# Kernel optimization log

Measured on AMD Instinct MI355X. Metric: run time of the kernel, lower is better.

Reference implementation:

```python
import jax, jax.numpy as jnp
import numpy as np

K = 75        # kpoints
L = 8         # number of labels (output_dim)


def _knn_nonconformity(q, t, train_label, k=K, num_labels=L):
    """Brute-force kNN (Euclidean) + distance-weighted nonconformity.
    q: [B, D] queries; t: [N, D] train bank; train_label: [N] int.
    Returns [B, num_labels]: for each class i, sum of 1/dist over the k
    nearest neighbors whose label != i (0 weight for zero distance)."""
    # squared distances [B, N]
    d2 = (jnp.sum(q * q, axis=1, keepdims=True)
          - 2.0 * q @ t.T
          + jnp.sum(t * t, axis=1)[None, :])
    d2 = jnp.maximum(d2, 0.0)
    neg_top, idx = jax.lax.top_k(-d2, k)          # k smallest d2
    dist = jnp.sqrt(jnp.maximum(-neg_top, 0.0))    # [B, k]
    safe = jnp.where(dist > 0, dist, 1.0)
    w = jnp.where(dist > 0, 1.0 / safe, 0.0)       # [B, k]
    mismatch = 1.0 - jax.nn.one_hot(train_label[idx], num_labels, dtype=w.dtype)  # [B,k,L]
    return jnp.einsum('bk,bkl->bl', w, mismatch)


def setup_inputs() -> dict:
    key = jax.random.key(0)
    ks = jax.random.split(key, 12)
    B, N, D, H, C = 1024, 50000, 83, 128, 10000
    s = lambda fan_in: 1.0 / np.sqrt(fan_in)
    return {
        'x': jax.random.normal(ks[0], (B, D), jnp.float32),
        'train_x': jax.random.normal(ks[1], (N, D), jnp.float32),
        'train_label': jax.random.randint(ks[2], (N,), 0, L, jnp.int32),
        'cali': jax.random.uniform(ks[3], (C,), jnp.float32) * 50.0,
        'W1': jax.random.normal(ks[4], (D, H), jnp.float32) * s(D),
        'b1': jnp.zeros((H,), jnp.float32),
        'W2': jax.random.normal(ks[5], (H, H), jnp.float32) * s(H),
        'b2': jnp.zeros((H,), jnp.float32),
        'W3': jax.random.normal(ks[6], (H, H), jnp.float32) * s(H),
        'b3': jnp.zeros((H,), jnp.float32),
        'W4': jax.random.normal(ks[7], (H, L), jnp.float32) * s(H),
        'b4': jnp.zeros((L,), jnp.float32),
    }


def reference(x, train_x, train_label, cali, W1, b1, W2, b2, W3, b3, W4, b4):
    relu = jax.nn.relu
    # query-side MLP (inference: dropout inactive)
    h1 = relu(x @ W1 + b1)
    h2 = relu(h1 @ W2 + b2)
    h3 = relu(h2 @ W3 + b3)
    out = jax.nn.softmax(h3 @ W4 + b4, axis=-1)
    # train-side feature banks (what each kNTree was fit on)
    t1 = relu(train_x @ W1 + b1)
    t2 = relu(t1 @ W2 + b2)
    t3 = relu(t2 @ W3 + b3)
    t4 = jax.nn.softmax(t3 @ W4 + b4, axis=-1)
    # per-layer nonconformity [B, L], summed across the 5 layers
    total = (_knn_nonconformity(x, train_x, train_label)
             + _knn_nonconformity(h1, t1, train_label)
             + _knn_nonconformity(h2, t2, train_label)
             + _knn_nonconformity(h3, t3, train_label)
             + _knn_nonconformity(out, t4, train_label))
    # empirical p-value: fraction of calibration scores >= total nonconformity
    counts = jnp.sum(cali[None, None, :] >= total[:, :, None], axis=-1)  # [B, L]
    return counts.astype(jnp.float32) / cali.shape[0]
```

## Files before the change

kernel.cpp:

```cpp
#include <hip/hip_runtime.h>
#include <math.h>

#define KNN 75
#define NL 8
#define NB 1024
#define NT 50000
#define NT_PAD 50048
#define NCALI 10000
#define KC 32
#define TT 128
#define NTB 391
#define SLOTS 16
#define CAP 6144
#define NSUB 2048
#define NSB 16
#define SSTRIDE 24
#define SOFF 11
#define RSEL 32
#define MLP8_BQ 1563

#define PB_Q    384
#define PB_BANK 18750
#define PB_W1   48
#define PB_W23  64
#define PREP_BLOCKS (PB_Q+PB_BANK+PB_W1+2*PB_W23)

typedef __attribute__((ext_vector_type(8))) short bf16x8;
typedef __attribute__((ext_vector_type(4))) float f32x4;

__device__ __forceinline__ int swz(int c){ return c + ((c>>5)<<2); }

__device__ __forceinline__ unsigned short f2bf_rn(float x){
  unsigned u = __float_as_uint(x);
  unsigned r = (u + 0x7FFFu + ((u>>16)&1u)) >> 16;
  return (unsigned short)r;
}
__device__ __forceinline__ float bf2f(unsigned short h){
  return __uint_as_float(((unsigned)h)<<16);
}
__device__ __forceinline__ bf16x8 ld8(const unsigned short* p){
  return *(const bf16x8*)p;
}
__device__ __forceinline__ void gl_lds16(const unsigned short* g, unsigned short* l){
  __builtin_amdgcn_global_load_lds(
      (const __attribute__((address_space(1))) void*)g,
      (__attribute__((address_space(3))) void*)l, 16, 0, 0);
}

__device__ __forceinline__ void pad_one(const float* __restrict__ in,
                                        float* __restrict__ out, int M,
                                        int Din, int Dout, int idx){
  if (idx >= M*Dout) return;
  int r = idx / Dout, c = idx - r*Dout;
  out[idx] = (c < Din) ? in[r*Din + c] : 0.f;
}
__device__ __forceinline__ void wsplit_one(const float* __restrict__ W, int kreal,
                                           int dp, unsigned short* __restrict__ WtH,
                                           unsigned short* __restrict__ WtL, int idx){
  int n = idx / dp, k = idx - n*dp;
  float v = (k < kreal) ? W[(size_t)k*128 + n] : 0.f;
  unsigned short h = f2bf_rn(v);
  WtH[idx] = h;
  WtL[idx] = f2bf_rn(v - bf2f(h));
}
__global__ void prep_k(const float* __restrict__ x, float* __restrict__ xq0,
                       const float* __restrict__ txr, float* __restrict__ tbA,
                       const float* __restrict__ W1, unsigned short* wt1H, unsigned short* wt1L,
                       const float* __restrict__ W2, unsigned short* wt2H, unsigned short* wt2L,
                       const float* __restrict__ W3, unsigned short* wt3H, unsigned short* wt3L){
  int b = blockIdx.x, tid = threadIdx.x;
  if (b < PB_Q){
    pad_one(x, xq0, NB, 83, 96, b*256 + tid);
  } else if (b < PB_Q + PB_BANK){
    pad_one(txr, tbA, NT, 83, 96, (b-PB_Q)*256 + tid);
  } else if (b < PB_Q + PB_BANK + PB_W1){
    wsplit_one(W1, 83, 96,  wt1H, wt1L, (b-PB_Q-PB_BANK)*256 + tid);
  } else if (b < PB_Q + PB_BANK + PB_W1 + PB_W23){
    wsplit_one(W2, 128, 128, wt2H, wt2L, (b-PB_Q-PB_BANK-PB_W1)*256 + tid);
  } else {
    wsplit_one(W3, 128, 128, wt3H, wt3L, (b-PB_Q-PB_BANK-PB_W1-PB_W23)*256 + tid);
  }
}

__global__ void mlp8sm_k(const float* __restrict__ AB, const float* __restrict__ AQ,
                         const float* __restrict__ W4, const float* __restrict__ b4,
                         float* __restrict__ OutB,
                         unsigned short* __restrict__ SBH, unsigned short* __restrict__ SBL,
                         float* __restrict__ nrmB,
                         float* __restrict__ OutQ,
                         unsigned short* __restrict__ SQH, unsigned short* __restrict__ SQL,
                         float* __restrict__ nrmQ){
  __shared__ float Ws[128*8];
  int tid = threadIdx.x;
  for (int i=tid;i<1024;i+=256) Ws[i]=W4[i];
  __syncthreads();
  int b = blockIdx.x;
  bool isq = (b >= MLP8_BQ);
  int r = (isq ? (b-MLP8_BQ) : b)*32 + (tid>>3), c = tid&7;
  int M = isq ? NB : NT;
  if (r >= M) return;
  const float* A = isq ? AQ : AB;
  float* Out = isq ? OutQ : OutB;
  unsigned short* SH = isq ? SQH : SBH;
  unsigned short* SL = isq ? SQL : SBL;
  float* nrm = isq ? nrmQ : nrmB;
  const float* a = &A[(size_t)r*128];
  float acc = b4[c];
  #pragma unroll 16
  for (int k=0;k<128;k++) acc += a[k]*Ws[k*8+c];
  int lane = tid & 63, base = lane & ~7;
  float v[8];
  #pragma unroll
  for (int j=0;j<8;j++) v[j] = __shfl(acc, base+j, 64);
  float m=-1e30f;
  #pragma unroll
  for (int j=0;j<8;j++) m = v[j]>m ? v[j] : m;
  float s=0.f;
  #pragma unroll
  for (int j=0;j<8;j++){ v[j]=__expf(v[j]-m); s+=v[j]; }
  float inv=1.f/s;
  float nn=0.f;
  #pragma unroll
  for (int j=0;j<8;j++){ float pv=v[j]*inv; v[j]=pv; nn+=pv*pv; }
  float* p = &Out[(size_t)r*32];
  float pv = v[c];
  p[c]    = pv;
  p[8+c]  = 0.f;
  p[16+c] = 0.f;
  p[24+c] = 0.f;
  unsigned short h = f2bf_rn(pv);
  SH[(size_t)r*32 + c]    = h;
  SL[(size_t)r*32 + c]    = f2bf_rn(pv - bf2f(h));
  SH[(size_t)r*32 + 8+c]  = 0; SL[(size_t)r*32 + 8+c]  = 0;
  SH[(size_t)r*32 + 16+c] = 0; SL[(size_t)r*32 + 16+c] = 0;
  SH[(size_t)r*32 + 24+c] = 0; SL[(size_t)r*32 + 24+c] = 0;
  if (c==0) nrm[r] = nn;
}

__global__ void conv_norm_k(
    const float* __restrict__ XA, unsigned short* __restrict__ HA,
    unsigned short* __restrict__ LA, float* __restrict__ nA, int MA,
    const float* __restrict__ XB, unsigned short* __restrict__ HB,
    unsigned short* __restrict__ LB, float* __restrict__ nB, int MB,
    int dp)
{
  int w = threadIdx.x>>6, lane = threadIdx.x&63;
  int row = blockIdx.x*4 + w;
  const float* src; unsigned short* dh; unsigned short* dl; float* nrm;
  if (row < MA){
    src=&XA[(size_t)row*dp]; dh=&HA[(size_t)row*dp]; dl=&LA[(size_t)row*dp]; nrm=&nA[row];
  } else {
    int r2 = row - MA;
    if (r2 >= MB) return;
    src=&XB[(size_t)r2*dp]; dh=&HB[(size_t)r2*dp]; dl=&LB[(size_t)r2*dp]; nrm=&nB[r2];
  }
  float s=0.f;
  for (int c=lane*2; c<dp; c+=128){
    float2 v = *(const float2*)&src[c];
    s += v.x*v.x + v.y*v.y;
    unsigned short h0 = f2bf_rn(v.x), h1 = f2bf_rn(v.y);
    float r0 = v.x - bf2f(h0), r1 = v.y - bf2f(h1);
    ushort2 hh; hh.x=h0; hh.y=h1;
    ushort2 ll; ll.x=f2bf_rn(r0); ll.y=f2bf_rn(r1);
    *(ushort2*)&dh[c]=hh;
    *(ushort2*)&dl[c]=ll;
  }
  #pragma unroll
  for (int off=32;off>0;off>>=1) s += __shfl_down(s, off, 64);
  if (lane==0) *nrm=s;
}

__device__ __forceinline__ void find_bin(int* hist, int* part, int nb, int Krem,
                                         int tid, int* s_B, int* s_lob){
  int ch = nb>>8;
  int base = tid*ch;
  int s=0;
  for (int b=base;b<base+ch;b++) s+=hist[b];
  int lane = tid & 63, wv = tid>>6;
  int v = s;
  #pragma unroll
  for (int off=1; off<64; off<<=1){
    int u = __shfl_up(v, off, 64);
    if (lane >= off) v += u;
  }
  if (lane==63) part[wv] = v;
  __syncthreads();
  int wbase = 0;
  #pragma unroll
  for (int w2=0; w2<4; w2++) wbase += (w2 < wv) ? part[w2] : 0;
  v += wbase;
  int excl = v - s;
  if (v >= Krem && excl < Krem){
    int lob = excl, B = base + ch - 1;
    for (int b=base;b<base+ch;b++){
      if (lob + hist[b] >= Krem){ B=b; break; }
      lob += hist[b];
    }
    *s_B = B; *s_lob = lob;
  }
  if (tid==255 && v < Krem){ *s_B = nb-1; *s_lob = 0; }
  __syncthreads();
}

__global__ __launch_bounds__(256) void sel64_k(const unsigned* __restrict__ skeys,
                                               unsigned* __restrict__ Tthr){
  __shared__ unsigned buf[NSUB];
  __shared__ int hist[2048];
  __shared__ int part[256];
  __shared__ int sB, sLob;
  int tid=threadIdx.x, q=blockIdx.x;
  for (int i=tid;i<NSUB;i+=256) buf[i]=skeys[(size_t)q*NSUB+i];
  int Krem=RSEL;
  for (int i=tid;i<2048;i+=256) hist[i]=0;
  __syncthreads();
  for (int i=tid;i<NSUB;i+=256) atomicAdd(&hist[buf[i]>>21],1);
  __syncthreads();
  find_bin(hist,part,2048,Krem,tid,&sB,&sLob);
  unsigned pre=(unsigned)sB; Krem-=sLob;
  for (int i=tid;i<2048;i+=256) hist[i]=0;
  __syncthreads();
  for (int i=tid;i<NSUB;i+=256){ unsigned k=buf[i]; if ((k>>21)==pre) atomicAdd(&hist[(k>>10)&0x7FFu],1); }
  __syncthreads();
  find_bin(hist,part,2048,Krem,tid,&sB,&sLob);
  pre=(pre<<11)|(unsigned)sB; Krem-=sLob;
  for (int i=tid;i<1024;i+=256) hist[i]=0;
  __syncthreads();
  for (int i=tid;i<NSUB;i+=256){ unsigned k=buf[i]; if ((k>>10)==pre) atomicAdd(&hist[k&0x3FFu],1); }
  __syncthreads();
  find_bin(hist,part,1024,Krem,tid,&sB,&sLob);
  if (tid==0) Tthr[q]=(pre<<10)|(unsigned)sB;
}

#define MFMA_SEC(BHC, BLC, AH, AL)                                               \
  _Pragma("unroll")                                                              \
  for (int tj=0;tj<8;tj++){                                                      \
    int rowB = tj*16 + col;                                                      \
    int sw = (((quad + (rowB>>1)) & 3) << 3);                                    \
    bf16x8 bh = *(const bf16x8*)&(BHC)[rowB*32 + sw];                            \
    bf16x8 bl = *(const bf16x8*)&(BLC)[rowB*32 + sw];                            \
    acc[tj] = __builtin_amdgcn_mfma_f32_16x16x32_bf16(AH, bh, acc[tj], 0,0,0);   \
    acc[tj] = __builtin_amdgcn_mfma_f32_16x16x32_bf16(AH, bl, acc[tj], 0,0,0);   \
    acc[tj] = __builtin_amdgcn_mfma_f32_16x16x32_bf16(AL, bh, acc[tj], 0,0,0);   \
  }

#define MFMA_KLOOP(ROWMAP)                                                       \
  size_t aoff = (size_t)(qbase + w*16 + col)*dp + quad*8;                        \
  const unsigned short* pAH = QH + aoff;                                         \
  const unsigned short* pAL = QL + aoff;                                         \
  int i0 = tid,      row0 = i0>>2, sg0 = ((i0&3) - (row0>>1)) & 3;               \
  int i1 = tid+256,  row1 = i1>>2, sg1 = ((i1&3) - (row1>>1)) & 3;               \
  size_t g0 = (size_t)(ROWMAP(n0+row0))*dp + (size_t)sg0*8;                      \
  size_t g1 = (size_t)(ROWMAP(n0+row1))*dp + (size_t)sg1*8;                      \
  f32x4 acc[8];                                                                  \
  _Pragma("unroll")                                                              \
  for (int tj=0;tj<8;tj++){ f32x4 z={0.f,0.f,0.f,0.f}; acc[tj]=z; }              \
  gl_lds16(TH + g0, BH0 + i0*8);                                                 \
  gl_lds16(TH + g1, BH0 + i1*8);                                                 \
  gl_lds16(TL + g0, BL0 + i0*8);                                                 \
  gl_lds16(TL + g1, BL0 + i1*8);                                                 \
  bf16x8 xh = ld8(pAH), xl = ld8(pAL);                                           \
  bf16x8 yh = xh, yl = xl;                                                       \
  _Pragma("unroll")                                                              \
  for (int kc=0; kc<kchunks; kc+=2){                                             \
    __syncthreads();                                                             \
    if (kc+1 < kchunks){                                                         \
      size_t ko=(size_t)(kc+1)*32;                                               \
      gl_lds16(TH + g0 + ko, BH1 + i0*8);                                        \
      gl_lds16(TH + g1 + ko, BH1 + i1*8);                                        \
      gl_lds16(TL + g0 + ko, BL1 + i0*8);                                        \
      gl_lds16(TL + g1 + ko, BL1 + i1*8);                                        \
      yh = ld8(pAH + ko); yl = ld8(pAL + ko);                                    \
    }                                                                            \
    MFMA_SEC(BH0, BL0, xh, xl);                                                  \
    if (kc+1 < kchunks){                                                         \
      __syncthreads();                                                           \
      if (kc+2 < kchunks){                                                       \
        size_t ko=(size_t)(kc+2)*32;                                             \
        gl_lds16(TH + g0 + ko, BH0 + i0*8);                                      \
        gl_lds16(TH + g1 + ko, BH0 + i1*8);                                      \
        gl_lds16(TL + g0 + ko, BL0 + i0*8);                                      \
        gl_lds16(TL + g1 + ko, BL0 + i1*8);                                      \
        xh = ld8(pAH + ko); xl = ld8(pAL + ko);                                  \
      }                                                                          \
      MFMA_SEC(BH1, BL1, yh, yl);                                                \
    }                                                                            \
  }

#define ROW_ID(r) (r)
#define ROW_SUB(r) ((r)*SSTRIDE + SOFF)

template<int KCH>
__global__ __launch_bounds__(256) void dist_mfma_k(
    const unsigned short* __restrict__ QH, const unsigned short* __restrict__ QL,
    const unsigned short* __restrict__ TH, const unsigned short* __restrict__ TL,
    const float* __restrict__ qn, const float* __restrict__ tn,
    const int* __restrict__ labels, const unsigned* __restrict__ Tthr,
    unsigned* __restrict__ slab)
{
  constexpr int dp = KCH*32;
  __shared__ __align__(16) unsigned short smem[4*4096];
  unsigned short* BH0 = smem;
  unsigned short* BH1 = smem + 4096;
  unsigned short* BL0 = smem + 8192;
  unsigned short* BL1 = smem + 12288;
  unsigned (*hitbuf)[SLOTS] = (unsigned (*)[SLOTS])smem;
  int* hcnt = (int*)(smem + 4096);
  int b = blockIdx.x;
  int xcd = b & 7, s = b >> 3;
  int qb = s & 15, tslot = s >> 4;
  int t_blk = xcd + 8*tslot;
  if (t_blk >= NTB) return;
  int tid = threadIdx.x, w = tid>>6, lane = tid&63;
  int quad = lane>>4, col = lane&15;
  int qbase = qb*64;
  int n0 = t_blk*TT;
  constexpr int kchunks = KCH;

  MFMA_KLOOP(ROW_ID)

  __syncthreads();
  if (tid<64) hcnt[tid]=0;
  __syncthreads();
  float qnr[4]; unsigned Tq[4]; float thrF[4];
  #pragma unroll
  for (int r=0;r<4;r++){
    int q = qbase + w*16 + quad*4 + r;
    qnr[r]  = qn[q];
    Tq[r]   = Tthr[q];
    thrF[r] = __uint_as_float(Tq[r] | 7u);
  }
  #pragma unroll
  for (int tj=0;tj<8;tj++){
    int t = n0 + tj*16 + col;
    if (t < NT){
      float tnv = tn[t];
      unsigned lab = (unsigned)labels[t];
      #pragma unroll
      for (int r=0;r<4;r++){
        float d2 = fmaf(-2.f, acc[tj][r], qnr[r] + tnv);
        if (d2 <= thrF[r]){
          float d2c = fmaxf(d2, 0.f);
          unsigned key = (__float_as_uint(d2c)&0xFFFFFFF8u) | lab;
          if (key < Tq[r]){
            int ql = w*16 + quad*4 + r;
            int idx = atomicAdd(&hcnt[ql], 1);
            if (idx < SLOTS-1) hitbuf[ql][1+idx] = key;
          }
        }
      }
    }
  }
  __syncthreads();
  if (tid<64) hitbuf[tid][0]=(unsigned)hcnt[tid];
  __syncthreads();
  {
    int q = tid>>2, sub = (tid&3)*4;
    uint4 v = *(uint4*)&hitbuf[q][sub];
    *(uint4*)&slab[((size_t)(qbase+q)*NTB + t_blk)*SLOTS + sub] = v;
  }
}

template<int KCH>
__global__ __launch_bounds__(256) void dist_sub_k(
    const unsigned short* __restrict__ QH, const unsigned short* __restrict__ QL,
    const unsigned short* __restrict__ TH, const unsigned short* __restrict__ TL,
    const float* __restrict__ qn, const float* __restrict__ tn,
    const int* __restrict__ labels, unsigned* __restrict__ keys)
{
  constexpr int dp = KCH*32;
  __shared__ __align__(16) unsigned short smem[4*4096];
  unsigned short* BH0 = smem;
  unsigned short* BH1 = smem + 4096;
  unsigned short* BL0 = smem + 8192;
  unsigned short* BL1 = smem + 12288;
  int b = blockIdx.x;
  int qb = b & 15, t_blk = b >> 4;
  int tid = threadIdx.x, w = tid>>6, lane = tid&63;
  int quad = lane>>4, col = lane&15;
  int qbase = qb*64;
  int n0 = t_blk*TT;
  constexpr int kchunks = KCH;

  MFMA_KLOOP(ROW_SUB)

  float qnr[4];
  #pragma unroll
  for (int r=0;r<4;r++)
    qnr[r] = qn[qbase + w*16 + quad*4 + r];
  #pragma unroll
  for (int tj=0;tj<8;tj++){
    int sI = n0 + tj*16 + col;
    int g  = sI*SSTRIDE + SOFF;
    float tnv = tn[g];
    unsigned lab = (unsigned)labels[g];
    #pragma unroll
    for (int r=0;r<4;r++){
      float d2 = fmaxf(fmaf(-2.f, acc[tj][r], qnr[r] + tnv), 0.f);
      unsigned key = (__float_as_uint(d2)&0xFFFFFFF8u) | lab;
      int q = qbase + w*16 + quad*4 + r;
      keys[(size_t)q*NSUB + sI] = key;
    }
  }
}

template<int KCH>
__global__ __launch_bounds__(256) void mlp_mfma_k(
    const unsigned short* __restrict__ bkH, const unsigned short* __restrict__ bkL,
    const unsigned short* __restrict__ qh,  const unsigned short* __restrict__ ql,
    const unsigned short* __restrict__ TH, const unsigned short* __restrict__ TL,
    const float* __restrict__ bias,
    float* __restrict__ OutB, unsigned short* __restrict__ SBH,
    unsigned short* __restrict__ SBL, float* __restrict__ nrmB,
    float* __restrict__ OutQ, unsigned short* __restrict__ SQH,
    unsigned short* __restrict__ SQL, float* __restrict__ nrmQ)
{
  constexpr int dp = KCH*32;
  __shared__ __align__(16) unsigned short smem[4*4096];
  unsigned short* BH0 = smem;
  unsigned short* BH1 = smem + 4096;
  unsigned short* BL0 = smem + 8192;
  unsigned short* BL1 = smem + 12288;
  int b = blockIdx.x;
  bool isq = (b >= 2*NTB);
  const unsigned short* QH = isq ? qh : bkH;
  const unsigned short* QL = isq ? ql : bkL;
  float* Out = isq ? OutQ : OutB;
  unsigned short* SH = isq ? SQH : SBH;
  unsigned short* SL = isq ? SQL : SBL;
  float* nrm = isq ? nrmQ : nrmB;
  int M = isq ? NB : NT;
  int tid = threadIdx.x, w = tid>>6, lane = tid&63;
  int quad = lane>>4, col = lane&15;
  int qbase = (isq ? (b - 2*NTB) : b) * 64;
  int n0 = 0;
  constexpr int kchunks = KCH;

  MFMA_KLOOP(ROW_ID)

  float bb[8];
  #pragma unroll
  for (int tj=0;tj<8;tj++) bb[tj] = bias[tj*16 + col];
  #pragma unroll
  for (int r=0;r<4;r++){
    int row = qbase + w*16 + quad*4 + r;
    if (row < M){
      float vv[8]; float s=0.f;
      #pragma unroll
      for (int tj=0;tj<8;tj++){
        float v = acc[tj][r] + bb[tj];
        v = v > 0.f ? v : 0.f;
        vv[tj] = v;
        s += v*v;
        Out[(size_t)row*128 + tj*16 + col] = v;
      }
      #pragma unroll
      for (int off=1; off<16; off<<=1) s += __shfl_xor(s, off, 16);
      if (col==0) nrm[row] = s;
      #pragma unroll
      for (int tj=0;tj<8;tj++){
        unsigned short h = f2bf_rn(vv[tj]);
        SH[(size_t)row*128 + tj*16 + col] = h;
        SL[(size_t)row*128 + tj*16 + col] = f2bf_rn(vv[tj] - bf2f(h));
      }
    }
  }
}

__global__ __launch_bounds__(256) void final_k(
    const unsigned* __restrict__ slab,
    const float* __restrict__ Qm, const float* __restrict__ Tm,
    const float* __restrict__ qn, const float* __restrict__ tn,
    const int* __restrict__ labels,
    float* __restrict__ tot, int first, int dp)
{
  __shared__ int hist[2048];
  __shared__ int part[256];
  __shared__ unsigned buf[CAP];
  __shared__ unsigned lowbuf[96];
  __shared__ float qrow[128];
  __shared__ int sB,sLob,s_cnt,s_low,s_bad;
  __shared__ float s_w[9];
  int tid=threadIdx.x, q=blockIdx.x;
  if (tid==0){ for (int j=0;j<9;j++) s_w[j]=0.f; s_cnt=0; s_low=0; s_bad=0; }
  __syncthreads();

  const unsigned* sq = slab + (size_t)q*NTB*SLOTS;
  for (int sidx=tid; sidx<NTB; sidx+=256){
    const unsigned* s = sq + (size_t)sidx*SLOTS;
    uint4 a = *(const uint4*)s;
    unsigned cnt = a.x;
    if (cnt > SLOTS-1){ s_bad=1; continue; }
    if (!cnt) continue;
    int base = atomicAdd(&s_cnt, (int)cnt);
    if (base + (int)cnt <= CAP){
      buf[base] = a.y;
      if (cnt>=2) buf[base+1] = a.z;
      if (cnt>=3) buf[base+2] = a.w;
      for (unsigned w=4; w<=cnt; w++) buf[base+w-1] = s[w];
    }
  }
  __syncthreads();
  int total = s_cnt;
  int bad = s_bad;

#define CONTRIB(kk) do{ float d2_=__uint_as_float((kk)&0xFFFFFFF8u); \
    if (d2_>0.f){ float w_=1.0f/sqrtf(d2_); \
      atomicAdd(&s_w[8],w_); atomicAdd(&s_w[(kk)&7u],w_); } }while(0)

  unsigned T; int Krem=KNN;
  if (!bad && total>=KNN && total<=CAP){
    for (int i=tid;i<2048;i+=256) hist[i]=0;
    __syncthreads();
    for (int i=tid;i<total;i+=256) atomicAdd(&hist[buf[i]>>21],1);
    __syncthreads();
    find_bin(hist,part,2048,Krem,tid,&sB,&sLob);
    unsigned pre=(unsigned)sB; Krem-=sLob;
    for (int i=tid;i<2048;i+=256) hist[i]=0;
    __syncthreads();
    for (int i=tid;i<total;i+=256){ unsigned k=buf[i]; if ((k>>21)==pre) atomicAdd(&hist[(k>>10)&0x7FFu],1); }
    __syncthreads();
    find_bin(hist,part,2048,Krem,tid,&sB,&sLob);
    pre=(pre<<11)|(unsigned)sB; Krem-=sLob;
    for (int i=tid;i<1024;i+=256) hist[i]=0;
    __syncthreads();
    for (int i=tid;i<total;i+=256){ unsigned k=buf[i]; if ((k>>10)==pre) atomicAdd(&hist[k&0x3FFu],1); }
    __syncthreads();
    find_bin(hist,part,1024,Krem,tid,&sB,&sLob);
    T=(pre<<10)|(unsigned)sB; Krem-=sLob;
    __syncthreads();
    for (int i=tid;i<total;i+=256){ unsigned k=buf[i]; if (k<T) CONTRIB(k); }
  } else {
    if (tid==0) s_cnt=0;
    for (int i=tid;i<dp;i+=256) qrow[i]=Qm[(size_t)q*dp+i];
    __syncthreads();
    float qq=qn[q];
    auto KEY=[&](int t)->unsigned{
      const float* br=&Tm[(size_t)t*dp];
      float dot=0.f;
      for (int k2=0;k2<dp;k2++) dot+=qrow[k2]*br[k2];
      float d2=fmaxf(qq-2.f*dot+tn[t],0.f);
      return (__float_as_uint(d2)&0xFFFFFFF8u)|(unsigned)labels[t];
    };
    for (int i=tid;i<2048;i+=256) hist[i]=0;
    __syncthreads();
    for (int t=tid;t<NT;t+=256) atomicAdd(&hist[KEY(t)>>21],1);
    __syncthreads();
    find_bin(hist,part,2048,Krem,tid,&sB,&sLob);
    int c=hist[sB]; Krem-=sLob;
    unsigned prefix=(unsigned)sB; int shift=21;
    if (c > CAP){
      __syncthreads();
      for (int i=tid;i<2048;i+=256) hist[i]=0;
      __syncthreads();
      for (int t=tid;t<NT;t+=256){ unsigned k=KEY(t); if ((k>>21)==prefix) atomicAdd(&hist[(k>>10)&0x7FFu],1); }
      __syncthreads();
      find_bin(hist,part,2048,Krem,tid,&sB,&sLob);
      c=hist[sB]; Krem-=sLob; prefix=(prefix<<11)|(unsigned)sB; shift=10;
    }
    if (c > CAP){
      __syncthreads();
      for (int i=tid;i<1024;i+=256) hist[i]=0;
      __syncthreads();
      for (int t=tid;t<NT;t+=256){ unsigned k=KEY(t); if ((k>>10)==prefix) atomicAdd(&hist[k&0x3FFu],1); }
      __syncthreads();
      find_bin(hist,part,1024,Krem,tid,&sB,&sLob);
      c=hist[sB]; Krem-=sLob; prefix=(prefix<<10)|(unsigned)sB; shift=0;
    }
    if (c <= CAP){
      for (int t=tid;t<NT;t+=256){
        unsigned k=KEY(t); unsigned pp=k>>shift;
        if (pp==prefix){ int j=atomicAdd(&s_cnt,1); if (j<CAP) buf[j]=k; }
        else if (pp<prefix){ int j=atomicAdd(&s_low,1); if (j<96) lowbuf[j]=k; }
      }
      __syncthreads();
      int sh=shift;
      while (sh>0){
        int nsh=(sh==21)?10:0;
        int nb=1<<(sh-nsh);
        __syncthreads();
        for (int i=tid;i<nb;i+=256) hist[i]=0;
        __syncthreads();
        int cc=s_cnt;
        for (int i=tid;i<cc;i+=256) atomicAdd(&hist[(buf[i]>>nsh)&(unsigned)(nb-1)],1);
        __syncthreads();
        find_bin(hist,part,nb,Krem,tid,&sB,&sLob);
        Krem-=sLob; prefix=(prefix<<(sh-nsh))|(unsigned)sB; sh=nsh;
      }
      T=prefix;
      __syncthreads();
      int lowc=s_low, cc=s_cnt;
      for (int i=tid;i<lowc;i+=256){ unsigned k=lowbuf[i]; CONTRIB(k); }
      for (int i=tid;i<cc;i+=256){ unsigned k=buf[i]; if (k<T) CONTRIB(k); }
    } else {
      T=prefix;
      for (int t=tid;t<NT;t+=256){ unsigned k=KEY(t); if (k<T) CONTRIB(k); }
    }
  }
  __syncthreads();
  if (tid==0){
    float d2=__uint_as_float(T&0xFFFFFFF8u);
    float w=(d2>0.f)?(1.0f/sqrtf(d2)):0.f;
    s_w[8] += (float)Krem*w;
    s_w[T&7u] += (float)Krem*w;
  }
  __syncthreads();
  if (tid<8){
    float contrib = s_w[8]-s_w[tid];
    size_t o=(size_t)q*NL+tid;
    tot[o] = first ? contrib : tot[o]+contrib;
  }
#undef CONTRIB
}

__global__ void pvalue_k(const float* __restrict__ tot, const float* __restrict__ cali,
                         float* __restrict__ out){
  __shared__ float t8[NL];
  __shared__ int part[4][NL];
  int tid=threadIdx.x, q=blockIdx.x;
  if (tid<NL) t8[tid]=tot[(size_t)q*NL+tid];
  __syncthreads();
  float th[NL];
  #pragma unroll
  for (int c=0;c<NL;c++) th[c]=t8[c];
  int cnt[NL];
  #pragma unroll
  for (int c=0;c<NL;c++) cnt[c]=0;
  for (int i=tid;i<NCALI;i+=256){
    float v=cali[i];
    #pragma unroll
    for (int c=0;c<NL;c++) cnt[c] += (v>=th[c]) ? 1 : 0;
  }
  #pragma unroll
  for (int c=0;c<NL;c++){
    #pragma unroll
    for (int off=32;off>0;off>>=1) cnt[c]+=__shfl_down(cnt[c],off,64);
  }
  if ((tid&63)==0){
    #pragma unroll
    for (int c=0;c<NL;c++) part[tid>>6][c]=cnt[c];
  }
  __syncthreads();
  if (tid<NL){
    int s=part[0][tid]+part[1][tid]+part[2][tid]+part[3][tid];
    out[(size_t)q*NL+tid] = (float)s / 10000.f;
  }
}

template<int KCH>
static void knn_layer(const float* Qm, const float* Bank,
                      const unsigned short* qh, const unsigned short* ql, float* qnl,
                      const unsigned short* bkH, const unsigned short* bkL,
                      int first, const int* lbl, float* tnb,
                      unsigned* skeys, unsigned* sT, unsigned* slab,
                      float* tot, hipStream_t stream){
  constexpr int dp = KCH*32;
  dist_sub_k<KCH><<<16*NSB,256,0,stream>>>(qh,ql,bkH,bkL,qnl,tnb,lbl,skeys);
  sel64_k<<<NB,256,0,stream>>>(skeys,sT);
  dist_mfma_k<KCH><<<8*16*49,256,0,stream>>>(qh,ql,bkH,bkL,qnl,tnb,lbl,sT,slab);
  final_k<<<NB,256,0,stream>>>(slab,Qm,Bank,qnl,tnb,lbl,tot,first,dp);
}

extern "C" void kernel_launch(void* const* d_in, const int* in_sizes, int n_in,
                              void* d_out, int out_size, void* d_ws, size_t ws_size,
                              hipStream_t stream) {
  const float* x   = (const float*)d_in[0];
  const float* txr = (const float*)d_in[1];
  const int*   lbl = (const int*)  d_in[2];
  const float* cal = (const float*)d_in[3];
  const float* W1  = (const float*)d_in[4];
  const float* b1  = (const float*)d_in[5];
  const float* W2  = (const float*)d_in[6];
  const float* b2  = (const float*)d_in[7];
  const float* W3  = (const float*)d_in[8];
  const float* b3  = (const float*)d_in[9];
  const float* W4  = (const float*)d_in[10];
  const float* b4  = (const float*)d_in[11];
  float* out = (float*)d_out;
  float* ws  = (float*)d_ws;

  size_t off=0;
  float* xq0=ws+off; off+=(size_t)NB*96;
  float* xq1=ws+off; off+=(size_t)NB*128;
  float* xq2=ws+off; off+=(size_t)NB*128;
  float* xq3=ws+off; off+=(size_t)NB*128;
  float* xq4=ws+off; off+=(size_t)NB*32;
  float* tbA=ws+off; off+=(size_t)NT*128;
  float* tbB=ws+off; off+=(size_t)NT*128;
  float* tb4=ws+off; off+=(size_t)NT*32;
  float* qnb=ws+off; off+=(size_t)5*NB;
  float* tnb=ws+off; off+=(size_t)NT;
  float* tot=ws+off; off+=(size_t)NB*NL;
  unsigned* sT=(unsigned*)(ws+off); off+=NB;
  unsigned short* qH0=(unsigned short*)(ws+off); off+=(size_t)NB*48;
  unsigned short* qL0=(unsigned short*)(ws+off); off+=(size_t)NB*48;
  unsigned short* qH1=(unsigned short*)(ws+off); off+=(size_t)NB*64;
  unsigned short* qL1=(unsigned short*)(ws+off); off+=(size_t)NB*64;
  unsigned short* qH2=(unsigned short*)(ws+off); off+=(size_t)NB*64;
  unsigned short* qL2=(unsigned short*)(ws+off); off+=(size_t)NB*64;
  unsigned short* qH3=(unsigned short*)(ws+off); off+=(size_t)NB*64;
  unsigned short* qL3=(unsigned short*)(ws+off); off+=(size_t)NB*64;
  unsigned short* qH4=(unsigned short*)(ws+off); off+=(size_t)NB*16;
  unsigned short* qL4=(unsigned short*)(ws+off); off+=(size_t)NB*16;
  unsigned short* bkAH=(unsigned short*)(ws+off); off+=(size_t)NT_PAD*64;
  unsigned short* bkAL=(unsigned short*)(ws+off); off+=(size_t)NT_PAD*64;
  unsigned short* bkBH=(unsigned short*)(ws+off); off+=(size_t)NT_PAD*64;
  unsigned short* bkBL=(unsigned short*)(ws+off); off+=(size_t)NT_PAD*64;
  unsigned short* wt1H=(unsigned short*)(ws+off); off+=(size_t)128*48;
  unsigned short* wt1L=(unsigned short*)(ws+off); off+=(size_t)128*48;
  unsigned short* wt2H=(unsigned short*)(ws+off); off+=(size_t)128*64;
  unsigned short* wt2L=(unsigned short*)(ws+off); off+=(size_t)128*64;
  unsigned short* wt3H=(unsigned short*)(ws+off); off+=(size_t)128*64;
  unsigned short* wt3L=(unsigned short*)(ws+off); off+=(size_t)128*64;
  off=(off+3)&~(size_t)3;
  unsigned* slab=(unsigned*)(ws+off);
  unsigned* skeys=(unsigned*)(ws+off);
  { size_t slab_sz=(size_t)NB*NTB*SLOTS, skey_sz=(size_t)NB*NSUB;
    off += (slab_sz > skey_sz ? slab_sz : skey_sz); }

  prep_k<<<PREP_BLOCKS,256,0,stream>>>(x,xq0,txr,tbA,
                                       W1,wt1H,wt1L,W2,wt2H,wt2L,W3,wt3H,wt3L);
  conv_norm_k<<<(NT+NB)/4,256,0,stream>>>(tbA, bkAH, bkAL, tnb, NT,
                                          xq0, qH0, qL0, qnb+0*NB, NB, 96);

  knn_layer<3>(xq0, tbA, qH0,qL0, qnb+0*NB, bkAH,bkAL, 1, lbl, tnb, skeys,sT,slab, tot, stream);
  mlp_mfma_k<3><<<2*NTB+16,256,0,stream>>>(bkAH,bkAL, qH0,qL0, wt1H,wt1L, b1,
                                           tbB,bkBH,bkBL,tnb, xq1,qH1,qL1,qnb+1*NB);
  knn_layer<4>(xq1, tbB, qH1,qL1, qnb+1*NB, bkBH,bkBL, 0, lbl, tnb, skeys,sT,slab, tot, stream);
  mlp_mfma_k<4><<<2*NTB+16,256,0,stream>>>(bkBH,bkBL, qH1,qL1, wt2H,wt2L, b2,
                                           tbA,bkAH,bkAL,tnb, xq2,qH2,qL2,qnb+2*NB);
  knn_layer<4>(xq2, tbA, qH2,qL2, qnb+2*NB, bkAH,bkAL, 0, lbl, tnb, skeys,sT,slab, tot, stream);
  mlp_mfma_k<4><<<2*NTB+16,256,0,stream>>>(bkAH,bkAL, qH2,qL2, wt3H,wt3L, b3,
                                           tbB,bkBH,bkBL,tnb, xq3,qH3,qL3,qnb+3*NB);
  knn_layer<4>(xq3, tbB, qH3,qL3, qnb+3*NB, bkBH,bkBL, 0, lbl, tnb, skeys,sT,slab, tot, stream);
  mlp8sm_k<<<MLP8_BQ+32,256,0,stream>>>(tbB, xq3, W4, b4,
                                        tb4,bkAH,bkAL,tnb, xq4,qH4,qL4,qnb+4*NB);
  knn_layer<1>(xq4, tb4, qH4,qL4, qnb+4*NB, bkAH,bkAL, 0, lbl, tnb, skeys,sT,slab, tot, stream);

  pvalue_k<<<NB,256,0,stream>>>(tot,cal,out);
}
```

Measured before the change: 647.6 us.

## Fuse independent kNN stages across layers into shared multi-role kernels

Turns the per-layer kernels into device bodies and adds a fused kernel that dispatches by block index to run one layer's final selection, the next layer's subsample distances, and the MLP step in a single launch. Independent work from adjacent layers now fills the GPU together instead of running serially. To make this legal it gives each layer its own train-norm buffer and separates the slab and subsample key buffers. This costs extra workspace and a larger shared-memory arena per block, which may lower occupancy for the smaller roles.

```diff
diff --git a/kernel.cpp b/kernel.cpp
--- a/kernel.cpp
+++ b/kernel.cpp
@@ -18,6 +18,8 @@
 #define SOFF 11
 #define RSEL 32
 #define MLP8_BQ 1563
+#define MLPB (2*NTB+16)
+#define ARENA 34816
 
 #define PB_Q    384
 #define PB_BANK 18750
@@ -80,61 +82,6 @@
   } else {
     wsplit_one(W3, 128, 128, wt3H, wt3L, (b-PB_Q-PB_BANK-PB_W1-PB_W23)*256 + tid);
   }
-}
-
-__global__ void mlp8sm_k(const float* __restrict__ AB, const float* __restrict__ AQ,
-                         const float* __restrict__ W4, const float* __restrict__ b4,
-                         float* __restrict__ OutB,
-                         unsigned short* __restrict__ SBH, unsigned short* __restrict__ SBL,
-                         float* __restrict__ nrmB,
-                         float* __restrict__ OutQ,
-                         unsigned short* __restrict__ SQH, unsigned short* __restrict__ SQL,
-                         float* __restrict__ nrmQ){
-  __shared__ float Ws[128*8];
-  int tid = threadIdx.x;
-  for (int i=tid;i<1024;i+=256) Ws[i]=W4[i];
-  __syncthreads();
-  int b = blockIdx.x;
-  bool isq = (b >= MLP8_BQ);
-  int r = (isq ? (b-MLP8_BQ) : b)*32 + (tid>>3), c = tid&7;
-  int M = isq ? NB : NT;
-  if (r >= M) return;
-  const float* A = isq ? AQ : AB;
-  float* Out = isq ? OutQ : OutB;
-  unsigned short* SH = isq ? SQH : SBH;
-  unsigned short* SL = isq ? SQL : SBL;
-  float* nrm = isq ? nrmQ : nrmB;
-  const float* a = &A[(size_t)r*128];
-  float acc = b4[c];
-  #pragma unroll 16
-  for (int k=0;k<128;k++) acc += a[k]*Ws[k*8+c];
-  int lane = tid & 63, base = lane & ~7;
-  float v[8];
-  #pragma unroll
-  for (int j=0;j<8;j++) v[j] = __shfl(acc, base+j, 64);
-  float m=-1e30f;
-  #pragma unroll
-  for (int j=0;j<8;j++) m = v[j]>m ? v[j] : m;
-  float s=0.f;
-  #pragma unroll
-  for (int j=0;j<8;j++){ v[j]=__expf(v[j]-m); s+=v[j]; }
-  float inv=1.f/s;
-  float nn=0.f;
-  #pragma unroll
-  for (int j=0;j<8;j++){ float pv=v[j]*inv; v[j]=pv; nn+=pv*pv; }
-  float* p = &Out[(size_t)r*32];
-  float pv = v[c];
-  p[c]    = pv;
-  p[8+c]  = 0.f;
-  p[16+c] = 0.f;
-  p[24+c] = 0.f;
-  unsigned short h = f2bf_rn(pv);
-  SH[(size_t)r*32 + c]    = h;
-  SL[(size_t)r*32 + c]    = f2bf_rn(pv - bf2f(h));
-  SH[(size_t)r*32 + 8+c]  = 0; SL[(size_t)r*32 + 8+c]  = 0;
-  SH[(size_t)r*32 + 16+c] = 0; SL[(size_t)r*32 + 16+c] = 0;
-  SH[(size_t)r*32 + 24+c] = 0; SL[(size_t)r*32 + 24+c] = 0;
-  if (c==0) nrm[r] = nn;
 }
 
 __global__ void conv_norm_k(
@@ -361,19 +308,17 @@
 }
 
 template<int KCH>
-__global__ __launch_bounds__(256) void dist_sub_k(
+__device__ __forceinline__ void distsub_body(char* smc, int b,
     const unsigned short* __restrict__ QH, const unsigned short* __restrict__ QL,
     const unsigned short* __restrict__ TH, const unsigned short* __restrict__ TL,
     const float* __restrict__ qn, const float* __restrict__ tn,
     const int* __restrict__ labels, unsigned* __restrict__ keys)
 {
   constexpr int dp = KCH*32;
-  __shared__ __align__(16) unsigned short smem[4*4096];
-  unsigned short* BH0 = smem;
-  unsigned short* BH1 = smem + 4096;
-  unsigned short* BL0 = smem + 8192;
-  unsigned short* BL1 = smem + 12288;
-  int b = blockIdx.x;
+  unsigned short* BH0 = (unsigned short*)smc;
+  unsigned short* BH1 = BH0 + 4096;
+  unsigned short* BL0 = BH0 + 8192;
+  unsigned short* BL1 = BH0 + 12288;
   int qb = b & 15, t_blk = b >> 4;
   int tid = threadIdx.x, w = tid>>6, lane = tid&63;
   int quad = lane>>4, col = lane&15;
@@ -404,7 +349,7 @@
 }
 
 template<int KCH>
-__global__ __launch_bounds__(256) void mlp_mfma_k(
+__device__ __forceinline__ void mlp_body(char* smc, int b,
     const unsigned short* __restrict__ bkH, const unsigned short* __restrict__ bkL,
     const unsigned short* __restrict__ qh,  const unsigned short* __restrict__ ql,
     const unsigned short* __restrict__ TH, const unsigned short* __restrict__ TL,
@@ -415,12 +360,10 @@
     unsigned short* __restrict__ SQL, float* __restrict__ nrmQ)
 {
   constexpr int dp = KCH*32;
-  __shared__ __align__(16) unsigned short smem[4*4096];
-  unsigned short* BH0 = smem;
-  unsigned short* BH1 = smem + 4096;
-  unsigned short* BL0 = smem + 8192;
-  unsigned short* BL1 = smem + 12288;
-  int b = blockIdx.x;
+  unsigned short* BH0 = (unsigned short*)smc;
+  unsigned short* BH1 = BH0 + 4096;
+  unsigned short* BL0 = BH0 + 8192;
+  unsigned short* BL1 = BH0 + 12288;
   bool isq = (b >= 2*NTB);
   const unsigned short* QH = isq ? qh : bkH;
   const unsigned short* QL = isq ? ql : bkL;
@@ -466,22 +409,90 @@
   }
 }
 
-__global__ __launch_bounds__(256) void final_k(
+template<int KCH>
+__global__ __launch_bounds__(256) void mlp_mfma_k(
+    const unsigned short* bkH, const unsigned short* bkL,
+    const unsigned short* qh,  const unsigned short* ql,
+    const unsigned short* TH, const unsigned short* TL,
+    const float* bias,
+    float* OutB, unsigned short* SBH, unsigned short* SBL, float* nrmB,
+    float* OutQ, unsigned short* SQH, unsigned short* SQL, float* nrmQ)
+{
+  __shared__ __align__(16) char smc[32768];
+  mlp_body<KCH>(smc, blockIdx.x, bkH,bkL,qh,ql,TH,TL,bias,
+                OutB,SBH,SBL,nrmB,OutQ,SQH,SQL,nrmQ);
+}
+
+__device__ __forceinline__ void mlp8_body(char* smc, int b,
+    const float* __restrict__ AB, const float* __restrict__ AQ,
+    const float* __restrict__ W4, const float* __restrict__ b4,
+    float* __restrict__ OutB, unsigned short* __restrict__ SBH,
+    unsigned short* __restrict__ SBL, float* __restrict__ nrmB,
+    float* __restrict__ OutQ, unsigned short* __restrict__ SQH,
+    unsigned short* __restrict__ SQL, float* __restrict__ nrmQ)
+{
+  float* Ws = (float*)smc;
+  int tid = threadIdx.x;
+  for (int i=tid;i<1024;i+=256) Ws[i]=W4[i];
+  __syncthreads();
+  bool isq = (b >= MLP8_BQ);
+  int r = (isq ? (b-MLP8_BQ) : b)*32 + (tid>>3), c = tid&7;
+  int M = isq ? NB : NT;
+  if (r >= M) return;
+  const float* A = isq ? AQ : AB;
+  float* Out = isq ? OutQ : OutB;
+  unsigned short* SH = isq ? SQH : SBH;
+  unsigned short* SL = isq ? SQL : SBL;
+  float* nrm = isq ? nrmQ : nrmB;
+  const float* a = &A[(size_t)r*128];
+  float acc = b4[c];
+  #pragma unroll 16
+  for (int k=0;k<128;k++) acc += a[k]*Ws[k*8+c];
+  int lane = tid & 63, base = lane & ~7;
+  float v[8];
+  #pragma unroll
+  for (int j=0;j<8;j++) v[j] = __shfl(acc, base+j, 64);
+  float m=-1e30f;
+  #pragma unroll
+  for (int j=0;j<8;j++) m = v[j]>m ? v[j] : m;
+  float s=0.f;
+  #pragma unroll
+  for (int j=0;j<8;j++){ v[j]=__expf(v[j]-m); s+=v[j]; }
+  float inv=1.f/s;
+  float nn=0.f;
+  #pragma unroll
+  for (int j=0;j<8;j++){ float pv=v[j]*inv; v[j]=pv; nn+=pv*pv; }
+  float* p = &Out[(size_t)r*32];
+  float pv = v[c];
+  p[c]    = pv;
+  p[8+c]  = 0.f;
+  p[16+c] = 0.f;
+  p[24+c] = 0.f;
+  unsigned short h = f2bf_rn(pv);
+  SH[(size_t)r*32 + c]    = h;
+  SL[(size_t)r*32 + c]    = f2bf_rn(pv - bf2f(h));
+  SH[(size_t)r*32 + 8+c]  = 0; SL[(size_t)r*32 + 8+c]  = 0;
+  SH[(size_t)r*32 + 16+c] = 0; SL[(size_t)r*32 + 16+c] = 0;
+  SH[(size_t)r*32 + 24+c] = 0; SL[(size_t)r*32 + 24+c] = 0;
+  if (c==0) nrm[r] = nn;
+}
+
+__device__ void final_body(char* sm, int q,
     const unsigned* __restrict__ slab,
     const float* __restrict__ Qm, const float* __restrict__ Tm,
     const float* __restrict__ qn, const float* __restrict__ tn,
     const int* __restrict__ labels,
     float* __restrict__ tot, int first, int dp)
 {
-  __shared__ int hist[2048];
-  __shared__ int part[256];
-  __shared__ unsigned buf[CAP];
-  __shared__ unsigned lowbuf[96];
-  __shared__ float qrow[128];
-  __shared__ int sB,sLob,s_cnt,s_low,s_bad;
-  __shared__ float s_w[9];
-  int tid=threadIdx.x, q=blockIdx.x;
-  if (tid==0){ for (int j=0;j<9;j++) s_w[j]=0.f; s_cnt=0; s_low=0; s_bad=0; }
+  int* hist = (int*)sm;
+  int* part = (int*)(sm+8192);
+  unsigned* buf = (unsigned*)(sm+9216);
+  unsigned* lowbuf = (unsigned*)(sm+33792);
+  float* qrow = (float*)(sm+34176);
+  int* s_i = (int*)(sm+34688);
+  float* s_w = (float*)(sm+34708);
+  int tid=threadIdx.x;
+  if (tid==0){ for (int j=0;j<9;j++) s_w[j]=0.f; s_i[2]=0; s_i[3]=0; s_i[4]=0; }
   __syncthreads();
 
   const unsigned* sq = slab + (size_t)q*NTB*SLOTS;
@@ -489,9 +500,9 @@
     const unsigned* s = sq + (size_t)sidx*SLOTS;
     uint4 a = *(const uint4*)s;
     unsigned cnt = a.x;
-    if (cnt > SLOTS-1){ s_bad=1; continue; }
+    if (cnt > SLOTS-1){ s_i[4]=1; continue; }
     if (!cnt) continue;
-    int base = atomicAdd(&s_cnt, (int)cnt);
+    int base = atomicAdd(&s_i[2], (int)cnt);
     if (base + (int)cnt <= CAP){
       buf[base] = a.y;
       if (cnt>=2) buf[base+1] = a.z;
@@ -500,8 +511,8 @@
     }
   }
   __syncthreads();
-  int total = s_cnt;
-  int bad = s_bad;
+  int total = s_i[2];
+  int bad = s_i[4];
 
 #define CONTRIB(kk) do{ float d2_=__uint_as_float((kk)&0xFFFFFFF8u); \
     if (d2_>0.f){ float w_=1.0f/sqrtf(d2_); \
@@ -513,24 +524,24 @@
     __syncthreads();
     for (int i=tid;i<total;i+=256) atomicAdd(&hist[buf[i]>>21],1);
     __syncthreads();
-    find_bin(hist,part,2048,Krem,tid,&sB,&sLob);
-    unsigned pre=(unsigned)sB; Krem-=sLob;
+    find_bin(hist,part,2048,Krem,tid,&s_i[0],&s_i[1]);
+    unsigned pre=(unsigned)s_i[0]; Krem-=s_i[1];
     for (int i=tid;i<2048;i+=256) hist[i]=0;
     __syncthreads();
     for (int i=tid;i<total;i+=256){ unsigned k=buf[i]; if ((k>>21)==pre) atomicAdd(&hist[(k>>10)&0x7FFu],1); }
     __syncthreads();
-    find_bin(hist,part,2048,Krem,tid,&sB,&sLob);
-    pre=(pre<<11)|(unsigned)sB; Krem-=sLob;
+    find_bin(hist,part,2048,Krem,tid,&s_i[0],&s_i[1]);
+    pre=(pre<<11)|(unsigned)s_i[0]; Krem-=s_i[1];
     for (int i=tid;i<1024;i+=256) hist[i]=0;
     __syncthreads();
     for (int i=tid;i<total;i+=256){ unsigned k=buf[i]; if ((k>>10)==pre) atomicAdd(&hist[k&0x3FFu],1); }
     __syncthreads();
-    find_bin(hist,part,1024,Krem,tid,&sB,&sLob);
-    T=(pre<<10)|(unsigned)sB; Krem-=sLob;
+    find_bin(hist,part,1024,Krem,tid,&s_i[0],&s_i[1]);
+    T=(pre<<10)|(unsigned)s_i[0]; Krem-=s_i[1];
     __syncthreads();
     for (int i=tid;i<total;i+=256){ unsigned k=buf[i]; if (k<T) CONTRIB(k); }
   } else {
-    if (tid==0) s_cnt=0;
+    if (tid==0) s_i[2]=0;
     for (int i=tid;i<dp;i+=256) qrow[i]=Qm[(size_t)q*dp+i];
     __syncthreads();
     float qq=qn[q];
@@ -545,17 +556,17 @@
     __syncthreads();
     for (int t=tid;t<NT;t+=256) atomicAdd(&hist[KEY(t)>>21],1);
     __syncthreads();
-    find_bin(hist,part,2048,Krem,tid,&sB,&sLob);
-    int c=hist[sB]; Krem-=sLob;
-    unsigned prefix=(unsigned)sB; int shift=21;
+    find_bin(hist,part,2048,Krem,tid,&s_i[0],&s_i[1]);
+    int c=hist[s_i[0]]; Krem-=s_i[1];
+    unsigned prefix=(unsigned)s_i[0]; int shift=21;
     if (c > CAP){
       __syncthreads();
       for (int i=tid;i<2048;i+=256) hist[i]=0;
       __syncthreads();
       for (int t=tid;t<NT;t+=256){ unsigned k=KEY(t); if ((k>>21)==prefix) atomicAdd(&hist[(k>>10)&0x7FFu],1); }
       __syncthreads();
-      find_bin(hist,part,2048,Krem,tid,&sB,&sLob);
-      c=hist[sB]; Krem-=sLob; prefix=(prefix<<11)|(unsigned)sB; shift=10;
+      find_bin(hist,part,2048,Krem,tid,&s_i[0],&s_i[1]);
+      c=hist[s_i[0]]; Krem-=s_i[1]; prefix=(prefix<<11)|(unsigned)s_i[0]; shift=10;
     }
     if (c > CAP){
       __syncthreads();
@@ -563,14 +574,14 @@
       __syncthreads();
       for (int t=tid;t<NT;t+=256){ unsigned k=KEY(t); if ((k>>10)==prefix) atomicAdd(&hist[k&0x3FFu],1); }
       __syncthreads();
-      find_bin(hist,part,1024,Krem,tid,&sB,&sLob);
-      c=hist[sB]; Krem-=sLob; prefix=(prefix<<10)|(unsigned)sB; shift=0;
+      find_bin(hist,part,1024,Krem,tid,&s_i[0],&s_i[1]);
+      c=hist[s_i[0]]; Krem-=s_i[1]; prefix=(prefix<<10)|(unsigned)s_i[0]; shift=0;
     }
     if (c <= CAP){
       for (int t=tid;t<NT;t+=256){
         unsigned k=KEY(t); unsigned pp=k>>shift;
-        if (pp==prefix){ int j=atomicAdd(&s_cnt,1); if (j<CAP) buf[j]=k; }
-        else if (pp<prefix){ int j=atomicAdd(&s_low,1); if (j<96) lowbuf[j]=k; }
+        if (pp==prefix){ int j=atomicAdd(&s_i[2],1); if (j<CAP) buf[j]=k; }
+        else if (pp<prefix){ int j=atomicAdd(&s_i[3],1); if (j<96) lowbuf[j]=k; }
       }
       __syncthreads();
       int sh=shift;
@@ -580,15 +591,15 @@
         __syncthreads();
         for (int i=tid;i<nb;i+=256) hist[i]=0;
         __syncthreads();
-        int cc=s_cnt;
+        int cc=s_i[2];
         for (int i=tid;i<cc;i+=256) atomicAdd(&hist[(buf[i]>>nsh)&(unsigned)(nb-1)],1);
         __syncthreads();
-        find_bin(hist,part,nb,Krem,tid,&sB,&sLob);
-        Krem-=sLob; prefix=(prefix<<(sh-nsh))|(unsigned)sB; sh=nsh;
+        find_bin(hist,part,nb,Krem,tid,&s_i[0],&s_i[1]);
+        Krem-=s_i[1]; prefix=(prefix<<(sh-nsh))|(unsigned)s_i[0]; sh=nsh;
       }
       T=prefix;
       __syncthreads();
-      int lowc=s_low, cc=s_cnt;
+      int lowc=s_i[3], cc=s_i[2];
       for (int i=tid;i<lowc;i+=256){ unsigned k=lowbuf[i]; CONTRIB(k); }
       for (int i=tid;i<cc;i+=256){ unsigned k=buf[i]; if (k<T) CONTRIB(k); }
     } else {
@@ -612,6 +623,51 @@
 #undef CONTRIB
 }
 
+__global__ __launch_bounds__(256) void final_k(
+    const unsigned* slab, const float* Qm, const float* Tm,
+    const float* qn, const float* tn, const int* labels,
+    float* tot, int first, int dp)
+{
+  __shared__ __align__(16) char sm[ARENA];
+  final_body(sm, blockIdx.x, slab, Qm, Tm, qn, tn, labels, tot, first, dp);
+}
+
+template<int KSUB, int KMLP, int M8>
+__global__ __launch_bounds__(256) void fused_k(
+    int nf,
+    const unsigned* slab, const float* Qm, const float* Tm,
+    const float* qnF, const float* tnF, float* tot, int first, int dpF,
+    const unsigned short* qhS, const unsigned short* qlS,
+    const unsigned short* bkHS, const unsigned short* bkLS,
+    const float* qnS, const float* tnS, unsigned* skeys,
+    const int* labels,
+    const unsigned short* bkHM, const unsigned short* bkLM,
+    const unsigned short* qhM, const unsigned short* qlM,
+    const unsigned short* wtH, const unsigned short* wtL, const float* bias,
+    float* OutB, unsigned short* SBH, unsigned short* SBL, float* nrmB,
+    float* OutQ, unsigned short* SQH, unsigned short* SQL, float* nrmQ,
+    const float* AB8, const float* AQ8, const float* W4, const float* b4)
+{
+  __shared__ __align__(16) char sm[ARENA];
+  int b = blockIdx.x;
+  if (b < nf){
+    final_body(sm, b, slab, Qm, Tm, qnF, tnF, labels, tot, first, dpF);
+    return;
+  }
+  b -= nf;
+  if (b < 16*NSB){
+    distsub_body<KSUB>(sm, b, qhS, qlS, bkHS, bkLS, qnS, tnS, labels, skeys);
+    return;
+  }
+  b -= 16*NSB;
+  if constexpr (KMLP > 0){
+    mlp_body<KMLP>(sm, b, bkHM,bkLM,qhM,qlM, wtH,wtL, bias,
+                   OutB,SBH,SBL,nrmB,OutQ,SQH,SQL,nrmQ);
+  } else if constexpr (M8){
+    mlp8_body(sm, b, AB8, AQ8, W4, b4, OutB,SBH,SBL,nrmB,OutQ,SQH,SQL,nrmQ);
+  }
+}
+
 __global__ void pvalue_k(const float* __restrict__ tot, const float* __restrict__ cali,
                          float* __restrict__ out){
   __shared__ float t8[NL];
@@ -644,20 +700,6 @@
     int s=part[0][tid]+part[1][tid]+part[2][tid]+part[3][tid];
     out[(size_t)q*NL+tid] = (float)s / 10000.f;
   }
-}
-
-template<int KCH>
-static void knn_layer(const float* Qm, const float* Bank,
-                      const unsigned short* qh, const unsigned short* ql, float* qnl,
-                      const unsigned short* bkH, const unsigned short* bkL,
-                      int first, const int* lbl, float* tnb,
-                      unsigned* skeys, unsigned* sT, unsigned* slab,
-                      float* tot, hipStream_t stream){
-  constexpr int dp = KCH*32;
-  dist_sub_k<KCH><<<16*NSB,256,0,stream>>>(qh,ql,bkH,bkL,qnl,tnb,lbl,skeys);
-  sel64_k<<<NB,256,0,stream>>>(skeys,sT);
-  dist_mfma_k<KCH><<<8*16*49,256,0,stream>>>(qh,ql,bkH,bkL,qnl,tnb,lbl,sT,slab);
-  final_k<<<NB,256,0,stream>>>(slab,Qm,Bank,qnl,tnb,lbl,tot,first,dp);
 }
 
 extern "C" void kernel_launch(void* const* d_in, const int* in_sizes, int n_in,
@@ -688,7 +730,7 @@
   float* tbB=ws+off; off+=(size_t)NT*128;
   float* tb4=ws+off; off+=(size_t)NT*32;
   float* qnb=ws+off; off+=(size_t)5*NB;
-  float* tnb=ws+off; off+=(size_t)NT;
+  float* tnb=ws+off; off+=(size_t)5*NT;
   float* tot=ws+off; off+=(size_t)NB*NL;
   unsigned* sT=(unsigned*)(ws+off); off+=NB;
   unsigned short* qH0=(unsigned short*)(ws+off); off+=(size_t)NB*48;
@@ -712,29 +754,66 @@
   unsigned short* wt3H=(unsigned short*)(ws+off); off+=(size_t)128*64;
   unsigned short* wt3L=(unsigned short*)(ws+off); off+=(size_t)128*64;
   off=(off+3)&~(size_t)3;
-  unsigned* slab=(unsigned*)(ws+off);
-  unsigned* skeys=(unsigned*)(ws+off);
-  { size_t slab_sz=(size_t)NB*NTB*SLOTS, skey_sz=(size_t)NB*NSUB;
-    off += (slab_sz > skey_sz ? slab_sz : skey_sz); }
+  unsigned* slab=(unsigned*)(ws+off); off+=(size_t)NB*NTB*SLOTS;
+  unsigned* skeys=(unsigned*)(ws+off); off+=(size_t)NB*NSUB;
+
+  float* tnb0=tnb, *tnb1=tnb+NT, *tnb2=tnb+2*NT, *tnb3=tnb+3*NT, *tnb4=tnb+4*NT;
 
   prep_k<<<PREP_BLOCKS,256,0,stream>>>(x,xq0,txr,tbA,
                                        W1,wt1H,wt1L,W2,wt2H,wt2L,W3,wt3H,wt3L);
-  conv_norm_k<<<(NT+NB)/4,256,0,stream>>>(tbA, bkAH, bkAL, tnb, NT,
+  conv_norm_k<<<(NT+NB)/4,256,0,stream>>>(tbA, bkAH, bkAL, tnb0, NT,
                                           xq0, qH0, qL0, qnb+0*NB, NB, 96);
 
-  knn_layer<3>(xq0, tbA, qH0,qL0, qnb+0*NB, bkAH,bkAL, 1, lbl, tnb, skeys,sT,slab, tot, stream);
-  mlp_mfma_k<3><<<2*NTB+16,256,0,stream>>>(bkAH,bkAL, qH0,qL0, wt1H,wt1L, b1,
-                                           tbB,bkBH,bkBL,tnb, xq1,qH1,qL1,qnb+1*NB);
-  knn_layer<4>(xq1, tbB, qH1,qL1, qnb+1*NB, bkBH,bkBL, 0, lbl, tnb, skeys,sT,slab, tot, stream);
-  mlp_mfma_k<4><<<2*NTB+16,256,0,stream>>>(bkBH,bkBL, qH1,qL1, wt2H,wt2L, b2,
-                                           tbA,bkAH,bkAL,tnb, xq2,qH2,qL2,qnb+2*NB);
-  knn_layer<4>(xq2, tbA, qH2,qL2, qnb+2*NB, bkAH,bkAL, 0, lbl, tnb, skeys,sT,slab, tot, stream);
-  mlp_mfma_k<4><<<2*NTB+16,256,0,stream>>>(bkAH,bkAL, qH2,qL2, wt3H,wt3L, b3,
-                                           tbB,bkBH,bkBL,tnb, xq3,qH3,qL3,qnb+3*NB);
-  knn_layer<4>(xq3, tbB, qH3,qL3, qnb+3*NB, bkBH,bkBL, 0, lbl, tnb, skeys,sT,slab, tot, stream);
-  mlp8sm_k<<<MLP8_BQ+32,256,0,stream>>>(tbB, xq3, W4, b4,
-                                        tb4,bkAH,bkAL,tnb, xq4,qH4,qL4,qnb+4*NB);
-  knn_layer<1>(xq4, tb4, qH4,qL4, qnb+4*NB, bkAH,bkAL, 0, lbl, tnb, skeys,sT,slab, tot, stream);
+  fused_k<3,3,0><<<16*NSB + MLPB,256,0,stream>>>(0,
+      nullptr,nullptr,nullptr,nullptr,nullptr,nullptr,0,0,
+      qH0,qL0, bkAH,bkAL, qnb+0*NB, tnb0, skeys, lbl,
+      bkAH,bkAL, qH0,qL0, wt1H,wt1L, b1,
+      tbB,bkBH,bkBL,tnb1, xq1,qH1,qL1,qnb+1*NB,
+      nullptr,nullptr,nullptr,nullptr);
+  sel64_k<<<NB,256,0,stream>>>(skeys,sT);
+  dist_mfma_k<3><<<8*16*49,256,0,stream>>>(qH0,qL0,bkAH,bkAL,qnb+0*NB,tnb0,lbl,sT,slab);
+
+  fused_k<4,0,0><<<NB + 16*NSB,256,0,stream>>>(NB,
+      slab, xq0, tbA, qnb+0*NB, tnb0, tot, 1, 96,
+      qH1,qL1, bkBH,bkBL, qnb+1*NB, tnb1, skeys, lbl,
+      nullptr,nullptr,nullptr,nullptr,nullptr,nullptr,nullptr,
+      nullptr,nullptr,nullptr,nullptr,nullptr,nullptr,nullptr,nullptr,
+      nullptr,nullptr,nullptr,nullptr);
+  mlp_mfma_k<4><<<MLPB,256,0,stream>>>(bkBH,bkBL, qH1,qL1, wt2H,wt2L, b2,
+                                       tbA,bkAH,bkAL,tnb2, xq2,qH2,qL2,qnb+2*NB);
+  sel64_k<<<NB,256,0,stream>>>(skeys,sT);
+  dist_mfma_k<4><<<8*16*49,256,0,stream>>>(qH1,qL1,bkBH,bkBL,qnb+1*NB,tnb1,lbl,sT,slab);
+
+  fused_k<4,0,0><<<NB + 16*NSB,256,0,stream>>>(NB,
+      slab, xq1, tbB, qnb+1*NB, tnb1, tot, 0, 128,
+      qH2,qL2, bkAH,bkAL, qnb+2*NB, tnb2, skeys, lbl,
+      nullptr,nullptr,nullptr,nullptr,nullptr,nullptr,nullptr,
+      nullptr,nullptr,nullptr,nullptr,nullptr,nullptr,nullptr,nullptr,
+      nullptr,nullptr,nullptr,nullptr);
+  mlp_mfma_k<4><<<MLPB,256,0,stream>>>(bkAH,bkAL, qH2,qL2, wt3H,wt3L, b3,
+                                       tbB,bkBH,bkBL,tnb3, xq3,qH3,qL3,qnb+3*NB);
+  sel64_k<<<NB,256,0,stream>>>(skeys,sT);
+  dist_mfma_k<4><<<8*16*49,256,0,stream>>>(qH2,qL2,bkAH,bkAL,qnb+2*NB,tnb2,lbl,sT,slab);
+
+  fused_k<4,0,1><<<NB + 16*NSB + MLP8_BQ+32,256,0,stream>>>(NB,
+      slab, xq2, tbA, qnb+2*NB, tnb2, tot, 0, 128,
+      qH3,qL3, bkBH,bkBL, qnb+3*NB, tnb3, skeys, lbl,
+      nullptr,nullptr,nullptr,nullptr,nullptr,nullptr,nullptr,
+      tb4,bkAH,bkAL,tnb4, xq4,qH4,qL4,qnb+4*NB,
+      tbB, xq3, W4, b4);
+  sel64_k<<<NB,256,0,stream>>>(skeys,sT);
+  dist_mfma_k<4><<<8*16*49,256,0,stream>>>(qH3,qL3,bkBH,bkBL,qnb+3*NB,tnb3,lbl,sT,slab);
+
+  fused_k<1,0,0><<<NB + 16*NSB,256,0,stream>>>(NB,
+      slab, xq3, tbB, qnb+3*NB, tnb3, tot, 0, 128,
+      qH4,qL4, bkAH,bkAL, qnb+4*NB, tnb4, skeys, lbl,
+      nullptr,nullptr,nullptr,nullptr,nullptr,nullptr,nullptr,
+      nullptr,nullptr,nullptr,nullptr,nullptr,nullptr,nullptr,nullptr,
+      nullptr,nullptr,nullptr,nullptr);
+  sel64_k<<<NB,256,0,stream>>>(skeys,sT);
+  dist_mfma_k<1><<<8*16*49,256,0,stream>>>(qH4,qL4,bkAH,bkAL,qnb+4*NB,tnb4,lbl,sT,slab);
+
+  final_k<<<NB,256,0,stream>>>(slab, xq4, tb4, qnb+4*NB, tnb4, lbl, tot, 0, 32);
 
   pvalue_k<<<NB,256,0,stream>>>(tot,cal,out);
 }
```

New measurement: 646.3 us. About the same (-0.2%).
